# Kernel optimization log

Hardware: AMD Instinct MI355X
Metric: run time of the kernel (lower is better)

The kernel has to match this reference:

```python
import jax, jax.numpy as jnp
import numpy as np

EPS = 1e-15
CLAMP = 1e-7


def _sqnorm(x):
    return jnp.sum(x * x, axis=-1, keepdims=True)


def _norm(x):
    return jnp.sqrt(jnp.maximum(_sqnorm(x), EPS))


def artanh(x):
    x = jnp.clip(x, -1.0 + CLAMP, 1.0 - CLAMP)
    return 0.5 * (jnp.log1p(x) - jnp.log1p(-x))


def expmap0(u):
    # Poincare ball, c = 1: exp map at origin
    n = _norm(u)
    return jnp.tanh(n) * u / n


def logmap0(p):
    n = _norm(p)
    return artanh(n) * p / n


def mobius_add(x, y):
    x2 = _sqnorm(x)
    y2 = _sqnorm(y)
    xy = jnp.sum(x * y, axis=-1, keepdims=True)
    num = (1.0 + 2.0 * xy + y2) * x + (1.0 - x2) * y
    den = 1.0 + 2.0 * xy + x2 * y2
    return num / jnp.maximum(den, EPS)


def expmap(u, p):
    # exp map of tangent u at ball point p
    n = _norm(u)
    lam = 2.0 / jnp.maximum(1.0 - _sqnorm(p), EPS)
    second = jnp.tanh(0.5 * lam * n) * u / n
    return mobius_add(p, second)


def ptransp0(x, u):
    # parallel transport of tangent u from origin to x: u * (lambda_0 / lambda_x)
    return u * (1.0 - _sqnorm(x))


def setup_inputs() -> dict:
    key = jax.random.key(0)
    k1, k2, k3, k4, k5, k6 = jax.random.split(key, 6)
    n_slot, n_int, d = 30000, 20000, 128
    n_edges, n_rel = 640000, 16
    n_nodes = n_slot + n_int
    return {
        "slot_embed": 0.05 * jax.random.normal(k1, (n_slot, d), dtype=jnp.float32),
        "int_embed": 0.05 * jax.random.normal(k2, (n_int, d), dtype=jnp.float32),
        "relation_embed": 0.05 * jax.random.normal(k3, (n_rel, d), dtype=jnp.float32),
        "src": jax.random.randint(k4, (n_edges,), 0, n_nodes, dtype=jnp.int64) if jax.config.jax_enable_x64 else jax.random.randint(k4, (n_edges,), 0, n_nodes, dtype=jnp.int32),
        "dst": jax.random.randint(k5, (n_edges,), 0, n_nodes, dtype=jnp.int32),
        "edge_type": jax.random.randint(k6, (n_edges,), 0, n_rel, dtype=jnp.int32),
    }


def reference(slot_embed, int_embed, relation_embed, src, dst, edge_type):
    n_slot = slot_embed.shape[0]
    n_nodes = n_slot + int_embed.shape[0]
    embed = jnp.concatenate([slot_embed, int_embed], axis=0)   # 'node'
    node1 = expmap0(embed)                                     # 'node1'

    # per-edge hyperbolic transform: gather src/dst/relation rows
    src_p = node1[src]                          # [E, d] point on ball
    tangent = embed[dst] + relation_embed[edge_type]  # [E, d] tangent at origin
    tan_sum = logmap0(expmap(ptransp0(src_p, tangent), src_p))  # [E, d]

    # g_inv reverses edges, so copy_e + mean aggregates onto original SRC nodes
    sums = jax.ops.segment_sum(tan_sum, src, num_segments=n_nodes)
    cnts = jax.ops.segment_sum(jnp.ones((src.shape[0],), tan_sum.dtype), src,
                               num_segments=n_nodes)
    out = sums / jnp.maximum(cnts, 1.0)[:, None]  # isolated nodes -> 0 (DGL mean)
    return out[:n_slot], out[n_slot:]
```

## Files before the change

kernel.cpp:

```cpp
#include <hip/hip_runtime.h>
#include <math.h>

#define EPSF 1e-15f
#define CLAMPF 1e-7f
#define D 128
#define ELLW 64

typedef float v2f __attribute__((ext_vector_type(2)));

__device__ __forceinline__ float rcpf(float x) { return __builtin_amdgcn_rcpf(x); }
__device__ __forceinline__ float rsqf(float x) { return __builtin_amdgcn_rsqf(x); }

__device__ __forceinline__ v2f vfma2(v2f a, v2f b, v2f c) {
#if __has_builtin(__builtin_elementwise_fma)
    return __builtin_elementwise_fma(a, b, c);
#else
    v2f r; r.x = fmaf(a.x, b.x, c.x); r.y = fmaf(a.y, b.y, c.y); return r;
#endif
}

__device__ __forceinline__ float tanh_fast2(float z2) {
    float e2 = __expf(z2);
    return 1.0f - 2.0f * rcpf(e2 + 1.0f);
}

template<int CTRL>
__device__ __forceinline__ float dpp_add(float v) {
    int s = __builtin_bit_cast(int, v);
    int m = __builtin_amdgcn_update_dpp(0, s, CTRL, 0xF, 0xF, true);
    return v + __builtin_bit_cast(float, m);
}
__device__ __forceinline__ float red16(float v) {
    v = dpp_add<0x128>(v);
    v = dpp_add<0x124>(v);
    v = dpp_add<0x122>(v);
    v = dpp_add<0x121>(v);
    return v;
}

struct v2x2 { v2f lo, hi; };
__device__ __forceinline__ v2x2 ld8(const float* p) {
    float4 f = *(const float4*)p;
    v2x2 r; r.lo = (v2f){f.x, f.y}; r.hi = (v2f){f.z, f.w}; return r;
}

__global__ void build_ell_kernel(const int* __restrict__ src,
                                 const int* __restrict__ dst,
                                 const int* __restrict__ etype,
                                 int* __restrict__ cnt,
                                 int* __restrict__ ell, int n_edges) {
    int i = blockIdx.x * blockDim.x + threadIdx.x;
    int base = i * 4;
    if (base >= n_edges) return;
    if (base + 4 <= n_edges) {
        int4 s = *(const int4*)(src + base);
        int4 d = *(const int4*)(dst + base);
        int4 e = *(const int4*)(etype + base);
        int p;
        p = atomicAdd(cnt + s.x, 1); if (p < ELLW) ell[s.x * ELLW + p] = d.x | (e.x << 20);
        p = atomicAdd(cnt + s.y, 1); if (p < ELLW) ell[s.y * ELLW + p] = d.y | (e.y << 20);
        p = atomicAdd(cnt + s.z, 1); if (p < ELLW) ell[s.z * ELLW + p] = d.z | (e.z << 20);
        p = atomicAdd(cnt + s.w, 1); if (p < ELLW) ell[s.w * ELLW + p] = d.w | (e.w << 20);
    } else {
        for (int k = base; k < n_edges; ++k) {
            int p = atomicAdd(cnt + src[k], 1);
            if (p < ELLW) ell[src[k] * ELLW + p] = dst[k] | (etype[k] << 20);
        }
    }
}

__global__ __launch_bounds__(256)
void node_agg_kernel(const float* __restrict__ slot,
                     const float* __restrict__ intm_virt,
                     const float* __restrict__ rel,
                     const int* __restrict__ ell,
                     const int* __restrict__ cnt,
                     float* __restrict__ out,
                     int n_slot, int n_nodes) {
    int wid  = (blockIdx.x * blockDim.x + threadIdx.x) >> 6;
    int lane = threadIdx.x & 63;
    if (wid >= n_nodes) return;
    int sl = lane & 15;
    int g  = lane >> 4;

    const float* xrow = ((wid < n_slot) ? slot : intm_virt) + (size_t)wid * D + sl * 8;
    v2x2 ea = ld8(xrow);
    v2x2 eb = ld8(xrow + 4);
    v2f ssv = ea.lo * ea.lo;
    ssv = vfma2(ea.hi, ea.hi, ssv);
    ssv = vfma2(eb.lo, eb.lo, ssv);
    ssv = vfma2(eb.hi, eb.hi, ssv);
    float ss = red16(ssv.x + ssv.y);

    float irn = rsqf(fmaxf(ss, EPSF));
    float n   = ss * irn;
    float thn = tanh_fast2(2.0f * n);
    float tf  = thn * irn;
    float x2  = thn * thn;
    v2f tfv = (v2f){tf, tf};
    v2f x0 = ea.lo * tfv, x1 = ea.hi * tfv;
    v2f x2v_ = eb.lo * tfv, x3 = eb.hi * tfv;

    float fac    = 1.0f - x2;
    float fac2   = fac * fac;
    float twoInv = 2.0f * rcpf(fmaxf(fac, EPSF));

    int cn = cnt[wid];
    int m  = (cn < ELLW) ? cn : ELLW;
    const int* erow = ell + (size_t)wid * ELLW;

    float accx = 0.0f;
    v2f ac0 = (v2f){0.f, 0.f}, ac1 = ac0, ac2 = ac0, ac3 = ac0;

    for (int p = 0; p < m; p += 4) {
        int ep = p + g;
        bool ok = ep < m;
        int pk = ok ? erow[ep] : 0;
        unsigned di = (unsigned)pk & 0xFFFFF;
        unsigned ri = ((unsigned)pk) >> 20;

        const float* drow = (((int)di < n_slot) ? slot : intm_virt)
                            + (size_t)di * D + sl * 8;
        const float* rrow = rel + (size_t)ri * D + sl * 8;
        v2x2 dv0 = ld8(drow);
        v2x2 dv1 = ld8(drow + 4);
        v2x2 rv0 = ld8(rrow);
        v2x2 rv1 = ld8(rrow + 4);

        v2f t0 = dv0.lo + rv0.lo;
        v2f t1 = dv0.hi + rv0.hi;
        v2f t2 = dv1.lo + rv1.lo;
        v2f t3 = dv1.hi + rv1.hi;

        v2f ttv = t0 * t0;
        ttv = vfma2(t1, t1, ttv);
        ttv = vfma2(t2, t2, ttv);
        ttv = vfma2(t3, t3, ttv);
        v2f xtv = x0 * t0;
        xtv = vfma2(x1, t1, xtv);
        xtv = vfma2(x2v_, t2, xtv);
        xtv = vfma2(x3, t3, xtv);

        float tt = red16(ttv.x + ttv.y);
        float xt = red16(xtv.x + xtv.y);

        float uu = fac2 * tt;
        float xu = fac * xt;

        float iru = rsqf(fmaxf(uu, EPSF));
        float nu  = uu * iru;
        float th  = tanh_fast2(nu * twoInv);
        float sc  = th * iru;
        float y2  = th * th;
        float xy  = sc * xu;
        float two_xy = xy + xy;
        float a    = 1.0f + two_xy + y2;
        float den  = fmaf(x2, y2, 1.0f + two_xy);
        float invden = rcpf(fmaxf(den, EPSF));
        float poly = fmaf(a * a, x2, fmaf(a * fac, two_xy, fac2 * y2));
        float qq   = invden * invden * poly;
        float irq  = rsqf(fmaxf(qq, EPSF));
        float nq   = qq * irq;
        float cl   = fminf(nq, 1.0f - CLAMPF);
        float at   = 0.5f * __logf((1.0f + cl) * rcpf(1.0f - cl));
        float sc2  = at * irq;
        float k    = sc2 * invden;
        float cx   = k * a;
        float ct   = k * sc * fac2;
        if (!ok) { cx = 0.0f; ct = 0.0f; }

        accx += cx;
        v2f ctv = (v2f){ct, ct};
        ac0 = vfma2(ctv, t0, ac0);
        ac1 = vfma2(ctv, t1, ac1);
        ac2 = vfma2(ctv, t2, ac2);
        ac3 = vfma2(ctv, t3, ac3);
    }

    float v0 = ac0.x, v1 = ac0.y, v2 = ac1.x, v3 = ac1.y;
    float v4 = ac2.x, v5 = ac2.y, v6 = ac3.x, v7 = ac3.y;
    #pragma unroll
    for (int d = 16; d < 64; d <<= 1) {
        accx += __shfl_xor(accx, d, 64);
        v0 += __shfl_xor(v0, d, 64);
        v1 += __shfl_xor(v1, d, 64);
        v2 += __shfl_xor(v2, d, 64);
        v3 += __shfl_xor(v3, d, 64);
        v4 += __shfl_xor(v4, d, 64);
        v5 += __shfl_xor(v5, d, 64);
        v6 += __shfl_xor(v6, d, 64);
        v7 += __shfl_xor(v7, d, 64);
    }

    if (lane < 16) {
        float invcnt = rcpf(fmaxf((float)cn, 1.0f));
        float4 w0 = make_float4((v0 + accx * x0.x) * invcnt,
                                (v1 + accx * x0.y) * invcnt,
                                (v2 + accx * x1.x) * invcnt,
                                (v3 + accx * x1.y) * invcnt);
        float4 w1 = make_float4((v4 + accx * x2v_.x) * invcnt,
                                (v5 + accx * x2v_.y) * invcnt,
                                (v6 + accx * x3.x) * invcnt,
                                (v7 + accx * x3.y) * invcnt);
        float* orow = out + (size_t)wid * D + sl * 8;
        *(float4*)(orow)     = w0;
        *(float4*)(orow + 4) = w1;
    }
}

extern "C" void kernel_launch(void* const* d_in, const int* in_sizes, int n_in,
                              void* d_out, int out_size, void* d_ws, size_t ws_size,
                              hipStream_t stream) {
    const float* slot = (const float*)d_in[0];
    const float* intm = (const float*)d_in[1];
    const float* rel  = (const float*)d_in[2];
    const int*   src  = (const int*)d_in[3];
    const int*   dst  = (const int*)d_in[4];
    const int*   etyp = (const int*)d_in[5];

    int n_slot  = in_sizes[0] / D;
    int n_int   = in_sizes[1] / D;
    int n_nodes = n_slot + n_int;
    int n_edges = in_sizes[3];

    float* out = (float*)d_out;
    const float* intm_virt = intm - (size_t)n_slot * D;

    int* cnt = (int*)d_ws;
    int* ell = cnt + n_nodes;

    hipMemsetAsync(cnt, 0, (size_t)n_nodes * sizeof(int), stream);

    {
        int threads = 256;
        int nthreads = (n_edges + 3) / 4;
        int blocks = (nthreads + threads - 1) / threads;
        build_ell_kernel<<<blocks, threads, 0, stream>>>(src, dst, etyp, cnt, ell,
                                                         n_edges);
    }
    {
        int threads = 256;
        int blocks = (n_nodes * 64 + threads - 1) / threads;
        node_agg_kernel<<<blocks, threads, 0, stream>>>(slot, intm_virt, rel, ell,
                                                        cnt, out, n_slot, n_nodes);
    }
}
```

Measured before the change: 93.63 us.

## Cache relation table in LDS, preload ELL row, simplify per-edge hyperbolic math

Each block now copies the relation embeddings into shared memory and reads them from there instead of from global memory. Each wave loads its whole ELL row once and hands entries to lane groups with shuffles, rather than doing a global load every iteration. The per-edge math is simplified algebraically: the fac scaling cancels, which removes a multiply and the twoInv reciprocal. The accx term is also folded into the accumulators before the cross-group reduction, saving one shuffle chain. The trade-offs are a block-wide barrier plus an LDS fill in every block, and a hard cap of 16 relations with no check on n_rel.

Measured after the change: 93.82 us. Within noise of the previous version (+0.2%).

```diff
diff --git a/kernel.cpp b/kernel.cpp
--- a/kernel.cpp
+++ b/kernel.cpp
@@ -5,6 +5,7 @@
 #define CLAMPF 1e-7f
 #define D 128
 #define ELLW 64
+#define MAXREL 16
 
 typedef float v2f __attribute__((ext_vector_type(2)));
 
@@ -27,7 +28,7 @@
 template<int CTRL>
 __device__ __forceinline__ float dpp_add(float v) {
     int s = __builtin_bit_cast(int, v);
-    int m = __builtin_amdgcn_update_dpp(0, s, CTRL, 0xF, 0xF, true);
+    int m = __builtin_amdgcn_update_dpp(s, s, CTRL, 0xF, 0xF, false);
     return v + __builtin_bit_cast(float, m);
 }
 __device__ __forceinline__ float red16(float v) {
@@ -76,7 +77,16 @@
                      const int* __restrict__ ell,
                      const int* __restrict__ cnt,
                      float* __restrict__ out,
-                     int n_slot, int n_nodes) {
+                     int n_slot, int n_nodes, int n_rel) {
+    __shared__ __align__(16) float rel_lds[MAXREL * D];
+    {
+        const float4* rs = (const float4*)rel;
+        float4* rd = (float4*)rel_lds;
+        int tot = n_rel * (D / 4);
+        for (int i = threadIdx.x; i < tot; i += 256) rd[i] = rs[i];
+    }
+    __syncthreads();
+
     int wid  = (blockIdx.x * blockDim.x + threadIdx.x) >> 6;
     int lane = threadIdx.x & 63;
     if (wid >= n_nodes) return;
@@ -101,31 +111,32 @@
     v2f x0 = ea.lo * tfv, x1 = ea.hi * tfv;
     v2f x2v_ = eb.lo * tfv, x3 = eb.hi * tfv;
 
-    float fac    = 1.0f - x2;
-    float fac2   = fac * fac;
-    float twoInv = 2.0f * rcpf(fmaxf(fac, EPSF));
+    float fac  = 1.0f - x2;
+    float fac2 = fac * fac;
 
     int cn = cnt[wid];
     int m  = (cn < ELLW) ? cn : ELLW;
     const int* erow = ell + (size_t)wid * ELLW;
 
+    int pk_all = (lane < m) ? erow[lane] : 0;
+
     float accx = 0.0f;
     v2f ac0 = (v2f){0.f, 0.f}, ac1 = ac0, ac2 = ac0, ac3 = ac0;
 
     for (int p = 0; p < m; p += 4) {
         int ep = p + g;
         bool ok = ep < m;
-        int pk = ok ? erow[ep] : 0;
+        int pk = __shfl(pk_all, ep & 63, 64);
         unsigned di = (unsigned)pk & 0xFFFFF;
         unsigned ri = ((unsigned)pk) >> 20;
 
         const float* drow = (((int)di < n_slot) ? slot : intm_virt)
                             + (size_t)di * D + sl * 8;
-        const float* rrow = rel + (size_t)ri * D + sl * 8;
+        const float* rl = rel_lds + ri * D + sl * 8;
         v2x2 dv0 = ld8(drow);
         v2x2 dv1 = ld8(drow + 4);
-        v2x2 rv0 = ld8(rrow);
-        v2x2 rv1 = ld8(rrow + 4);
+        v2x2 rv0 = ld8(rl);
+        v2x2 rv1 = ld8(rl + 4);
 
         v2f t0 = dv0.lo + rv0.lo;
         v2f t1 = dv0.hi + rv0.hi;
@@ -144,18 +155,16 @@
         float tt = red16(ttv.x + ttv.y);
         float xt = red16(xtv.x + xtv.y);
 
-        float uu = fac2 * tt;
-        float xu = fac * xt;
-
-        float iru = rsqf(fmaxf(uu, EPSF));
-        float nu  = uu * iru;
-        float th  = tanh_fast2(nu * twoInv);
-        float sc  = th * iru;
+        float irt = rsqf(fmaxf(tt, EPSF));
+        float st2 = 2.0f * tt * irt;
+        float th  = tanh_fast2(st2);
+        float w   = th * irt;
         float y2  = th * th;
-        float xy  = sc * xu;
+        float xy  = w * xt;
         float two_xy = xy + xy;
-        float a    = 1.0f + two_xy + y2;
-        float den  = fmaf(x2, y2, 1.0f + two_xy);
+        float opx = 1.0f + two_xy;
+        float a   = opx + y2;
+        float den = fmaf(x2, y2, opx);
         float invden = rcpf(fmaxf(den, EPSF));
         float poly = fmaf(a * a, x2, fmaf(a * fac, two_xy, fac2 * y2));
         float qq   = invden * invden * poly;
@@ -166,7 +175,7 @@
         float sc2  = at * irq;
         float k    = sc2 * invden;
         float cx   = k * a;
-        float ct   = k * sc * fac2;
+        float ct   = k * w * fac;
         if (!ok) { cx = 0.0f; ct = 0.0f; }
 
         accx += cx;
@@ -177,11 +186,16 @@
         ac3 = vfma2(ctv, t3, ac3);
     }
 
+    v2f axv = (v2f){accx, accx};
+    ac0 = vfma2(axv, x0, ac0);
+    ac1 = vfma2(axv, x1, ac1);
+    ac2 = vfma2(axv, x2v_, ac2);
+    ac3 = vfma2(axv, x3, ac3);
+
     float v0 = ac0.x, v1 = ac0.y, v2 = ac1.x, v3 = ac1.y;
     float v4 = ac2.x, v5 = ac2.y, v6 = ac3.x, v7 = ac3.y;
     #pragma unroll
     for (int d = 16; d < 64; d <<= 1) {
-        accx += __shfl_xor(accx, d, 64);
         v0 += __shfl_xor(v0, d, 64);
         v1 += __shfl_xor(v1, d, 64);
         v2 += __shfl_xor(v2, d, 64);
@@ -194,14 +208,8 @@
 
     if (lane < 16) {
         float invcnt = rcpf(fmaxf((float)cn, 1.0f));
-        float4 w0 = make_float4((v0 + accx * x0.x) * invcnt,
-                                (v1 + accx * x0.y) * invcnt,
-                                (v2 + accx * x1.x) * invcnt,
-                                (v3 + accx * x1.y) * invcnt);
-        float4 w1 = make_float4((v4 + accx * x2v_.x) * invcnt,
-                                (v5 + accx * x2v_.y) * invcnt,
-                                (v6 + accx * x3.x) * invcnt,
-                                (v7 + accx * x3.y) * invcnt);
+        float4 w0 = make_float4(v0 * invcnt, v1 * invcnt, v2 * invcnt, v3 * invcnt);
+        float4 w1 = make_float4(v4 * invcnt, v5 * invcnt, v6 * invcnt, v7 * invcnt);
         float* orow = out + (size_t)wid * D + sl * 8;
         *(float4*)(orow)     = w0;
         *(float4*)(orow + 4) = w1;
@@ -220,6 +228,7 @@
 
     int n_slot  = in_sizes[0] / D;
     int n_int   = in_sizes[1] / D;
+    int n_rel   = in_sizes[2] / D;
     int n_nodes = n_slot + n_int;
     int n_edges = in_sizes[3];
 
@@ -242,6 +251,7 @@
         int threads = 256;
         int blocks = (n_nodes * 64 + threads - 1) / threads;
         node_agg_kernel<<<blocks, threads, 0, stream>>>(slot, intm_virt, rel, ell,
-                                                        cnt, out, n_slot, n_nodes);
-    }
-}
+                                                        cnt, out, n_slot, n_nodes,
+                                                        n_rel);
+    }
+}
```
